# Kernel optimization log

Hardware: AMD Instinct MI355X
Metric: run time of the kernel (lower is better)

Reference implementation:

```python
import jax, jax.numpy as jnp
import numpy as np

B, S, D = 2, 2048, 512
H = 8
HD = D // H  # head dim = 64


def setup_inputs() -> dict:
    key = jax.random.key(0)
    ks = jax.random.split(key, 4)
    scale = 1.0 / np.sqrt(D)
    x = jax.random.normal(ks[0], (B, S, D), dtype=jnp.float32)
    wq = jax.random.normal(ks[1], (D, D), dtype=jnp.float32) * scale
    wk = jax.random.normal(ks[2], (D, D), dtype=jnp.float32) * scale
    wv = jax.random.normal(ks[3], (D, D), dtype=jnp.float32) * scale
    bq = jnp.zeros((D,), dtype=jnp.float32)
    bk = jnp.zeros((D,), dtype=jnp.float32)
    bv = jnp.zeros((D,), dtype=jnp.float32)
    return {"x": x, "wq": wq, "bq": bq, "wk": wk, "bk": bk, "wv": wv, "bv": bv}


def reference(x, wq, bq, wk, bk, wv, bv):
    # Linear projections (torch Linear: y = x @ W^T + b; weights here stored as [out,in])
    q = x @ wq.T + bq  # [B,S,D]
    k = x @ wk.T + bk
    v = x @ wv.T + bv
    # split heads -> [B,H,S,HD]
    q = q.reshape(B, S, H, HD).transpose(0, 2, 1, 3)
    k = k.reshape(B, S, H, HD).transpose(0, 2, 1, 3)
    v = v.reshape(B, S, H, HD).transpose(0, 2, 1, 3)
    # QK^T scores, scaled by 1/sqrt(head_dim)
    scores = jnp.einsum("bhqd,bhkd->bhqk", q, k) / jnp.sqrt(jnp.float32(HD))
    # softmax-free: elementwise sigmoid instead of softmax normalization
    attn = jax.nn.sigmoid(scores)  # [B,H,S,S] — the memory-bound intermediate
    out = jnp.einsum("bhqk,bhkd->bhqd", attn, v)
    # merge heads -> [B,S,D]
    return out.transpose(0, 2, 1, 3).reshape(B, S, D)
```

## Files before the change

### kernel.cpp

```cpp
#include <hip/hip_runtime.h>
#include <cstdint>
#include <cstddef>

#define BB   2
#define SS   2048
#define DD   512
#define HH   8
#define HDIM 64

typedef __attribute__((ext_vector_type(8)))  short          s16x8;
typedef __attribute__((ext_vector_type(8)))  unsigned short u16x8;
typedef __attribute__((ext_vector_type(16))) float          f32x16;

static __device__ __forceinline__ unsigned short f2bf(float f) {
  union { float f; unsigned u; } x; x.f = f;
  unsigned r = x.u + 0x7fffu + ((x.u >> 16) & 1u);
  return (unsigned short)(r >> 16);
}
static __device__ __forceinline__ unsigned packtrunc(float lo, float hi) {
  return __builtin_amdgcn_perm(__float_as_uint(hi), __float_as_uint(lo), 0x07060302u);
}

#define QSCALE (-0.18033688011111543f)

__global__ __launch_bounds__(256) void proj_kernel(
    const float* __restrict__ x,
    const float* __restrict__ wq, const float* __restrict__ wk, const float* __restrict__ wv,
    const float* __restrict__ bq, const float* __restrict__ bk, const float* __restrict__ bv,
    unsigned short* __restrict__ qo, unsigned short* __restrict__ ko,
    unsigned short* __restrict__ vt) {
  __shared__ unsigned short As[2][64 * 40];
  __shared__ unsigned short Bs[2][64 * 40];

  const int z = blockIdx.z;
  const float* w; const float* bias;
  if (z == 0)      { w = wq; bias = bq; }
  else if (z == 1) { w = wk; bias = bk; }
  else             { w = wv; bias = bv; }

  const int t = threadIdx.x;
  const int lane = t & 63, wave = t >> 6;
  const int ln = lane & 31, hi = lane >> 5;
  const int wr = wave >> 1, wc = wave & 1;
  const int m0 = blockIdx.x * 64, n0 = blockIdx.y * 64;

  float4 ar[2], br[2];
#pragma unroll
  for (int i = 0; i < 2; i++) {
    int c = t + i * 256;
    ar[i] = *(const float4*)&x[(size_t)(m0 + (c >> 3)) * DD + (c & 7) * 4];
    br[i] = *(const float4*)&w[(size_t)(n0 + (c >> 3)) * DD + (c & 7) * 4];
  }
#pragma unroll
  for (int i = 0; i < 2; i++) {
    int c = t + i * 256;
    uint2 ua, ub;
    ua.x = packtrunc(ar[i].x, ar[i].y); ua.y = packtrunc(ar[i].z, ar[i].w);
    ub.x = packtrunc(br[i].x, br[i].y); ub.y = packtrunc(br[i].z, br[i].w);
    *(uint2*)&As[0][(c >> 3) * 40 + (c & 7) * 4] = ua;
    *(uint2*)&Bs[0][(c >> 3) * 40 + (c & 7) * 4] = ub;
  }
  __syncthreads();

  f32x16 acc = {};

#pragma unroll 2
  for (int kt = 0; kt < 16; kt++) {
    const int cur = kt & 1, nxt = cur ^ 1;
    if (kt < 15) {
      int k0 = (kt + 1) * 32;
#pragma unroll
      for (int i = 0; i < 2; i++) {
        int c = t + i * 256;
        ar[i] = *(const float4*)&x[(size_t)(m0 + (c >> 3)) * DD + k0 + (c & 7) * 4];
        br[i] = *(const float4*)&w[(size_t)(n0 + (c >> 3)) * DD + k0 + (c & 7) * 4];
      }
    }
#pragma unroll
    for (int c = 0; c < 2; c++) {
      s16x8 af = *(const s16x8*)&As[cur][(wr * 32 + ln) * 40 + c * 16 + hi * 8];
      s16x8 bf = *(const s16x8*)&Bs[cur][(wc * 32 + ln) * 40 + c * 16 + hi * 8];
      acc = __builtin_amdgcn_mfma_f32_32x32x16_bf16(af, bf, acc, 0, 0, 0);
    }
    if (kt < 15) {
#pragma unroll
      for (int i = 0; i < 2; i++) {
        int c = t + i * 256;
        uint2 ua, ub;
        ua.x = packtrunc(ar[i].x, ar[i].y); ua.y = packtrunc(ar[i].z, ar[i].w);
        ub.x = packtrunc(br[i].x, br[i].y); ub.y = packtrunc(br[i].z, br[i].w);
        *(uint2*)&As[nxt][(c >> 3) * 40 + (c & 7) * 4] = ua;
        *(uint2*)&Bs[nxt][(c >> 3) * 40 + (c & 7) * 4] = ub;
      }
    }
    __syncthreads();
  }

  const int h = blockIdx.y;
  const int bidx = m0 >> 11;
  const int sbase = (m0 & 2047) + wr * 32;
  const int hd = wc * 32 + ln;
  const float bval = bias[n0 + hd];
  const size_t bhb = (size_t)(bidx * HH + h) * SS * HDIM;

  if (z == 0) {
#pragma unroll
    for (int r = 0; r < 16; r++) {
      int s = sbase + (r & 3) + 8 * (r >> 2) + 4 * hi;
      qo[bhb + (size_t)s * HDIM + hd] = f2bf((acc[r] + bval) * QSCALE);
    }
  } else if (z == 1) {
    const int c = hd >> 4, hk = (hd >> 3) & 1, j = hd & 7;
    const int kts = sbase >> 5;
    unsigned short* kd = ko + bhb + ((size_t)kts * 4 + c) * 512 + j;
#pragma unroll
    for (int r = 0; r < 16; r++) {
      int off = (r & 3) + 8 * (r >> 2) + 4 * hi;
      kd[(hk * 32 + off) * 8] = f2bf(acc[r] + bval);
    }
  } else {
    const int kts = sbase >> 5;
    unsigned short* vd = vt + bhb + ((size_t)kts * 4 + wc * 2) * 512 + ln * 8 + 4 * hi;
#pragma unroll
    for (int g = 0; g < 4; g++) {
      unsigned short* vg = vd + ((g >> 1) * 512) + (g & 1) * 256;
#pragma unroll
      for (int j = 0; j < 4; j += 2) {
        unsigned pk = (unsigned)f2bf(acc[g * 4 + j] + bval) |
                      ((unsigned)f2bf(acc[g * 4 + j + 1] + bval) << 16);
        *(unsigned*)&vg[j] = pk;
      }
    }
  }
}

__global__ __launch_bounds__(256, 2) void attn_kernel(
    const unsigned short* __restrict__ qb,
    const unsigned short* __restrict__ kfb,
    const unsigned short* __restrict__ vfb,
    float* __restrict__ out) {
  __shared__ __align__(16) float red[2 * 4096];

  const int t = threadIdx.x;
  const int lane = t & 63, wave = t >> 6;
  const int ln = lane & 31, hi = lane >> 5;
  const int fid = blockIdx.y * 32 + blockIdx.x;
  const int bh = fid & 15, qx = fid >> 4;
  const int b = bh >> 3, h = bh & 7;
  const unsigned short* qp = qb + (size_t)bh * SS * HDIM;
  const unsigned short* kfp = kfb + (size_t)bh * SS * HDIM;
  const unsigned short* vfp = vfb + (size_t)bh * SS * HDIM;
  const int q0 = qx * 64;

  s16x8 qf[2][4];
#pragma unroll
  for (int qs = 0; qs < 2; qs++)
#pragma unroll
    for (int c = 0; c < 4; c++)
      qf[qs][c] = *(const s16x8*)&qp[(size_t)(q0 + qs * 32 + ln) * HDIM + c * 16 + hi * 8];

  f32x16 o00 = {}, o01 = {}, o10 = {}, o11 = {};

  s16x8 kf[2][4], vf[2][4];
  int foff = wave * 4 * 512 + lane * 8;
#pragma unroll
  for (int c = 0; c < 4; c++) {
    kf[0][c] = *(const s16x8*)&kfp[foff + c * 512];
    vf[0][c] = *(const s16x8*)&vfp[foff + c * 512];
  }
  foff += 8192;

#pragma unroll 2
  for (int i = 0; i < 16; i++) {
    const int cur = i & 1, nxt = cur ^ 1;
    if (i < 15) {
#pragma unroll
      for (int c = 0; c < 4; c++) {
        kf[nxt][c] = *(const s16x8*)&kfp[foff + c * 512];
        vf[nxt][c] = *(const s16x8*)&vfp[foff + c * 512];
      }
      foff += 8192;
    }

    f32x16 st0 = {}, st1 = {};
#pragma unroll
    for (int c = 0; c < 4; c++) {
      st0 = __builtin_amdgcn_mfma_f32_32x32x16_bf16(kf[cur][c], qf[0][c], st0, 0, 0, 0);
      st1 = __builtin_amdgcn_mfma_f32_32x32x16_bf16(kf[cur][c], qf[1][c], st1, 0, 0, 0);
    }

    unsigned pgx[2][4], pgy[2][4];
#pragma unroll
    for (int qs = 0; qs < 2; qs++) {
      f32x16 stq = qs ? st1 : st0;
#pragma unroll
      for (int g = 0; g < 4; g++) {
        float p0 = __builtin_amdgcn_rcpf(1.0f + __builtin_amdgcn_exp2f(stq[4 * g + 0]));
        float p1 = __builtin_amdgcn_rcpf(1.0f + __builtin_amdgcn_exp2f(stq[4 * g + 1]));
        float p2 = __builtin_amdgcn_rcpf(1.0f + __builtin_amdgcn_exp2f(stq[4 * g + 2]));
        float p3 = __builtin_amdgcn_rcpf(1.0f + __builtin_amdgcn_exp2f(stq[4 * g + 3]));
        pgx[qs][g] = packtrunc(p0, p1);
        pgy[qs][g] = packtrunc(p2, p3);
      }
    }

#pragma unroll
    for (int c = 0; c < 2; c++) {
      const int gk = 2 * c + hi, gs = 2 * c + (hi ^ 1);
#pragma unroll
      for (int qs = 0; qs < 2; qs++) {
        unsigned rx = __shfl_xor((int)pgx[qs][gs], 32, 64);
        unsigned ry = __shfl_xor((int)pgy[qs][gs], 32, 64);
        union { unsigned u[4]; s16x8 v; } pu;
        pu.u[0] = hi ? rx : pgx[qs][gk];
        pu.u[1] = hi ? ry : pgy[qs][gk];
        pu.u[2] = hi ? pgx[qs][gk] : rx;
        pu.u[3] = hi ? pgy[qs][gk] : ry;
        if (qs == 0) {
          o00 = __builtin_amdgcn_mfma_f32_32x32x16_bf16(pu.v, vf[cur][c], o00, 0, 0, 0);
          o01 = __builtin_amdgcn_mfma_f32_32x32x16_bf16(pu.v, vf[cur][2 + c], o01, 0, 0, 0);
        } else {
          o10 = __builtin_amdgcn_mfma_f32_32x32x16_bf16(pu.v, vf[cur][c], o10, 0, 0, 0);
          o11 = __builtin_amdgcn_mfma_f32_32x32x16_bf16(pu.v, vf[cur][2 + c], o11, 0, 0, 0);
        }
      }
    }
  }

  if (wave >= 2) {
#pragma unroll
    for (int qs = 0; qs < 2; qs++)
#pragma unroll
      for (int dh = 0; dh < 2; dh++) {
        f32x16 ov = qs ? (dh ? o11 : o10) : (dh ? o01 : o00);
#pragma unroll
        for (int r = 0; r < 16; r++) {
          int ql = qs * 32 + (r & 3) + 8 * (r >> 2) + 4 * hi;
          red[(wave - 2) * 4096 + ql * 64 + dh * 32 + ln] = ov[r];
        }
      }
  }
  __syncthreads();
  if (wave < 2) {
#pragma unroll
    for (int qs = 0; qs < 2; qs++)
#pragma unroll
      for (int dh = 0; dh < 2; dh++) {
        f32x16 ov = qs ? (dh ? o11 : o10) : (dh ? o01 : o00);
#pragma unroll
        for (int r = 0; r < 16; r++) {
          int ql = qs * 32 + (r & 3) + 8 * (r >> 2) + 4 * hi;
          int idx = wave * 4096 + ql * 64 + dh * 32 + ln;
          red[idx] += ov[r];
        }
      }
  }
  __syncthreads();
  const float4* r0 = (const float4*)red;
  const float4* r1 = (const float4*)(red + 4096);
#pragma unroll
  for (int j = 0; j < 4; j++) {
    int g = t + j * 256;
    float4 s0 = r0[g], s1 = r1[g];
    float4 s;
    s.x = s0.x + s1.x; s.y = s0.y + s1.y; s.z = s0.z + s1.z; s.w = s0.w + s1.w;
    int q = g >> 4, dbase = (g & 15) * 4;
    *(float4*)&out[((size_t)(b * SS + q0 + q)) * DD + h * HDIM + dbase] = s;
  }
}

extern "C" void kernel_launch(void* const* d_in, const int* in_sizes, int n_in,
                              void* d_out, int out_size, void* d_ws, size_t ws_size,
                              hipStream_t stream) {
  const float* x  = (const float*)d_in[0];
  const float* wq = (const float*)d_in[1];
  const float* bq = (const float*)d_in[2];
  const float* wk = (const float*)d_in[3];
  const float* bk = (const float*)d_in[4];
  const float* wv = (const float*)d_in[5];
  const float* bv = (const float*)d_in[6];
  float* out = (float*)d_out;

  constexpr size_t XN = (size_t)BB * SS * DD;

  unsigned short* qo = (unsigned short*)d_ws;
  unsigned short* ko = qo + XN;
  unsigned short* vt = ko + XN;

  proj_kernel<<<dim3(64, 8, 3), 256, 0, stream>>>(x, wq, wk, wv, bq, bk, bv, qo, ko, vt);
  attn_kernel<<<dim3(SS / 64, BB * HH), 256, 0, stream>>>(qo, ko, vt, out);
}
```

Before: 133.2 us.

## Halve attention query tile and relayout V to drop cross-lane shuffles

```diff
diff --git a/kernel.cpp b/kernel.cpp
--- a/kernel.cpp
+++ b/kernel.cpp
@@ -9,7 +9,6 @@
 #define HDIM 64
 
 typedef __attribute__((ext_vector_type(8)))  short          s16x8;
-typedef __attribute__((ext_vector_type(8)))  unsigned short u16x8;
 typedef __attribute__((ext_vector_type(16))) float          f32x16;
 
 static __device__ __forceinline__ unsigned short f2bf(float f) {
@@ -120,10 +119,10 @@
     }
   } else {
     const int kts = sbase >> 5;
-    unsigned short* vd = vt + bhb + ((size_t)kts * 4 + wc * 2) * 512 + ln * 8 + 4 * hi;
+    unsigned short* vd = vt + bhb + ((size_t)kts * 4 + wc * 2) * 512 + hi * 256 + ln * 8;
 #pragma unroll
     for (int g = 0; g < 4; g++) {
-      unsigned short* vg = vd + ((g >> 1) * 512) + (g & 1) * 256;
+      unsigned short* vg = vd + (g >> 1) * 512 + (g & 1) * 4;
 #pragma unroll
       for (int j = 0; j < 4; j += 2) {
         unsigned pk = (unsigned)f2bf(acc[g * 4 + j] + bval) |
@@ -139,27 +138,25 @@
     const unsigned short* __restrict__ kfb,
     const unsigned short* __restrict__ vfb,
     float* __restrict__ out) {
-  __shared__ __align__(16) float red[2 * 4096];
+  __shared__ __align__(16) float red[2][2048];
 
   const int t = threadIdx.x;
   const int lane = t & 63, wave = t >> 6;
   const int ln = lane & 31, hi = lane >> 5;
-  const int fid = blockIdx.y * 32 + blockIdx.x;
+  const int fid = blockIdx.y * 64 + blockIdx.x;
   const int bh = fid & 15, qx = fid >> 4;
   const int b = bh >> 3, h = bh & 7;
   const unsigned short* qp = qb + (size_t)bh * SS * HDIM;
   const unsigned short* kfp = kfb + (size_t)bh * SS * HDIM;
   const unsigned short* vfp = vfb + (size_t)bh * SS * HDIM;
-  const int q0 = qx * 64;
-
-  s16x8 qf[2][4];
-#pragma unroll
-  for (int qs = 0; qs < 2; qs++)
-#pragma unroll
-    for (int c = 0; c < 4; c++)
-      qf[qs][c] = *(const s16x8*)&qp[(size_t)(q0 + qs * 32 + ln) * HDIM + c * 16 + hi * 8];
-
-  f32x16 o00 = {}, o01 = {}, o10 = {}, o11 = {};
+  const int q0 = qx * 32;
+
+  s16x8 qf[4];
+#pragma unroll
+  for (int c = 0; c < 4; c++)
+    qf[c] = *(const s16x8*)&qp[(size_t)(q0 + ln) * HDIM + c * 16 + hi * 8];
+
+  f32x16 o0 = {}, o1 = {};
 
   s16x8 kf[2][4], vf[2][4];
   int foff = wave * 4 * 512 + lane * 8;
@@ -182,84 +179,62 @@
       foff += 8192;
     }
 
-    f32x16 st0 = {}, st1 = {};
-#pragma unroll
-    for (int c = 0; c < 4; c++) {
-      st0 = __builtin_amdgcn_mfma_f32_32x32x16_bf16(kf[cur][c], qf[0][c], st0, 0, 0, 0);
-      st1 = __builtin_amdgcn_mfma_f32_32x32x16_bf16(kf[cur][c], qf[1][c], st1, 0, 0, 0);
-    }
-
-    unsigned pgx[2][4], pgy[2][4];
-#pragma unroll
-    for (int qs = 0; qs < 2; qs++) {
-      f32x16 stq = qs ? st1 : st0;
-#pragma unroll
-      for (int g = 0; g < 4; g++) {
-        float p0 = __builtin_amdgcn_rcpf(1.0f + __builtin_amdgcn_exp2f(stq[4 * g + 0]));
-        float p1 = __builtin_amdgcn_rcpf(1.0f + __builtin_amdgcn_exp2f(stq[4 * g + 1]));
-        float p2 = __builtin_amdgcn_rcpf(1.0f + __builtin_amdgcn_exp2f(stq[4 * g + 2]));
-        float p3 = __builtin_amdgcn_rcpf(1.0f + __builtin_amdgcn_exp2f(stq[4 * g + 3]));
-        pgx[qs][g] = packtrunc(p0, p1);
-        pgy[qs][g] = packtrunc(p2, p3);
-      }
+    f32x16 st = {};
+#pragma unroll
+    for (int c = 0; c < 4; c++)
+      st = __builtin_amdgcn_mfma_f32_32x32x16_bf16(kf[cur][c], qf[c], st, 0, 0, 0);
+
+    unsigned pg[8];
+#pragma unroll
+    for (int g = 0; g < 4; g++) {
+      float p0 = __builtin_amdgcn_rcpf(1.0f + __builtin_amdgcn_exp2f(st[4 * g + 0]));
+      float p1 = __builtin_amdgcn_rcpf(1.0f + __builtin_amdgcn_exp2f(st[4 * g + 1]));
+      float p2 = __builtin_amdgcn_rcpf(1.0f + __builtin_amdgcn_exp2f(st[4 * g + 2]));
+      float p3 = __builtin_amdgcn_rcpf(1.0f + __builtin_amdgcn_exp2f(st[4 * g + 3]));
+      pg[2 * g]     = packtrunc(p0, p1);
+      pg[2 * g + 1] = packtrunc(p2, p3);
     }
 
 #pragma unroll
     for (int c = 0; c < 2; c++) {
-      const int gk = 2 * c + hi, gs = 2 * c + (hi ^ 1);
-#pragma unroll
-      for (int qs = 0; qs < 2; qs++) {
-        unsigned rx = __shfl_xor((int)pgx[qs][gs], 32, 64);
-        unsigned ry = __shfl_xor((int)pgy[qs][gs], 32, 64);
-        union { unsigned u[4]; s16x8 v; } pu;
-        pu.u[0] = hi ? rx : pgx[qs][gk];
-        pu.u[1] = hi ? ry : pgy[qs][gk];
-        pu.u[2] = hi ? pgx[qs][gk] : rx;
-        pu.u[3] = hi ? pgy[qs][gk] : ry;
-        if (qs == 0) {
-          o00 = __builtin_amdgcn_mfma_f32_32x32x16_bf16(pu.v, vf[cur][c], o00, 0, 0, 0);
-          o01 = __builtin_amdgcn_mfma_f32_32x32x16_bf16(pu.v, vf[cur][2 + c], o01, 0, 0, 0);
-        } else {
-          o10 = __builtin_amdgcn_mfma_f32_32x32x16_bf16(pu.v, vf[cur][c], o10, 0, 0, 0);
-          o11 = __builtin_amdgcn_mfma_f32_32x32x16_bf16(pu.v, vf[cur][2 + c], o11, 0, 0, 0);
-        }
-      }
+      union { unsigned u[4]; s16x8 v; } pu;
+      pu.u[0] = pg[4 * c + 0];
+      pu.u[1] = pg[4 * c + 1];
+      pu.u[2] = pg[4 * c + 2];
+      pu.u[3] = pg[4 * c + 3];
+      o0 = __builtin_amdgcn_mfma_f32_32x32x16_bf16(pu.v, vf[cur][c], o0, 0, 0, 0);
+      o1 = __builtin_amdgcn_mfma_f32_32x32x16_bf16(pu.v, vf[cur][2 + c], o1, 0, 0, 0);
     }
   }
 
   if (wave >= 2) {
 #pragma unroll
-    for (int qs = 0; qs < 2; qs++)
-#pragma unroll
-      for (int dh = 0; dh < 2; dh++) {
-        f32x16 ov = qs ? (dh ? o11 : o10) : (dh ? o01 : o00);
-#pragma unroll
-        for (int r = 0; r < 16; r++) {
-          int ql = qs * 32 + (r & 3) + 8 * (r >> 2) + 4 * hi;
-          red[(wave - 2) * 4096 + ql * 64 + dh * 32 + ln] = ov[r];
-        }
-      }
+    for (int dh = 0; dh < 2; dh++) {
+      f32x16 ov = dh ? o1 : o0;
+#pragma unroll
+      for (int r = 0; r < 16; r++) {
+        int ql = (r & 3) + 8 * (r >> 2) + 4 * hi;
+        red[wave - 2][ql * 64 + dh * 32 + ln] = ov[r];
+      }
+    }
   }
   __syncthreads();
   if (wave < 2) {
 #pragma unroll
-    for (int qs = 0; qs < 2; qs++)
-#pragma unroll
-      for (int dh = 0; dh < 2; dh++) {
-        f32x16 ov = qs ? (dh ? o11 : o10) : (dh ? o01 : o00);
-#pragma unroll
-        for (int r = 0; r < 16; r++) {
-          int ql = qs * 32 + (r & 3) + 8 * (r >> 2) + 4 * hi;
-          int idx = wave * 4096 + ql * 64 + dh * 32 + ln;
-          red[idx] += ov[r];
-        }
-      }
+    for (int dh = 0; dh < 2; dh++) {
+      f32x16 ov = dh ? o1 : o0;
+#pragma unroll
+      for (int r = 0; r < 16; r++) {
+        int ql = (r & 3) + 8 * (r >> 2) + 4 * hi;
+        red[wave][ql * 64 + dh * 32 + ln] += ov[r];
+      }
+    }
   }
   __syncthreads();
-  const float4* r0 = (const float4*)red;
-  const float4* r1 = (const float4*)(red + 4096);
-#pragma unroll
-  for (int j = 0; j < 4; j++) {
+  const float4* r0 = (const float4*)&red[0][0];
+  const float4* r1 = (const float4*)&red[1][0];
+#pragma unroll
+  for (int j = 0; j < 2; j++) {
     int g = t + j * 256;
     float4 s0 = r0[g], s1 = r1[g];
     float4 s;
@@ -288,5 +263,5 @@
   unsigned short* vt = ko + XN;
 
   proj_kernel<<<dim3(64, 8, 3), 256, 0, stream>>>(x, wq, wk, wv, bq, bk, bv, qo, ko, vt);
-  attn_kernel<<<dim3(SS / 64, BB * HH), 256, 0, stream>>>(qo, ko, vt, out);
-}
+  attn_kernel<<<dim3(SS / 32, BB * HH), 256, 0, stream>>>(qo, ko, vt, out);
+}
```

Result: faster. 117.3 us (-12.0%).
